# Kernel tuning notes

Measured on AMD Instinct MI355X. Metric: run time of the kernel, lower is better.

Reference implementation:

```python
import jax, jax.numpy as jnp
import numpy as np

EPS = 1e-8

def setup_inputs() -> dict:
    key = jax.random.key(0)
    k1, k2 = jax.random.split(key)
    B, N, D, K = 8, 8192, 768, 256
    x = jax.random.normal(k1, (B, N, D), dtype=jnp.float32)
    centers = jax.random.normal(k2, (B, K, D), dtype=jnp.float32)
    return {"x": x, "centers": centers}

def reference(x, centers):
    # tokens_norm / centers_norm as in the torch module (add-eps normalization)
    tn = x / (jnp.linalg.norm(x, axis=-1, keepdims=True) + EPS)
    cn = centers / (jnp.linalg.norm(centers, axis=-1, keepdims=True) + EPS)
    # F.cosine_similarity re-normalizes with clamp(norm, min=eps)
    tn2 = tn / jnp.maximum(jnp.linalg.norm(tn, axis=-1, keepdims=True), EPS)
    cn2 = cn / jnp.maximum(jnp.linalg.norm(cn, axis=-1, keepdims=True), EPS)
    # fused: cosine similarity via plain matmul instead of (B,N,K,D) broadcast
    cos_sim = jnp.einsum('bnd,bkd->bnk', tn2, cn2)  # (B,N,K)
    dist = 1.0 - cos_sim
    prob = jax.nn.softmax(-dist, axis=-1)  # softmax over K
    # weighted aggregation over N: (B,K,D)
    num = jnp.einsum('bnk,bnd->bkd', prob, x)
    den = jnp.sum(prob, axis=1)[..., None] + EPS  # (B,K,1)
    return num / den
```

## Files before the change

### kernel.cpp

```cpp
#include <hip/hip_runtime.h>
#include <hip/hip_bf16.h>

typedef __attribute__((ext_vector_type(8))) short bf16x8;
typedef __attribute__((ext_vector_type(4))) float f32x4;
typedef unsigned short u16;
typedef unsigned int u32;

__device__ __forceinline__ u16 f2bf(float f) {
    u32 u = __float_as_uint(f);
    u = (u + 0x7FFFu + ((u >> 16) & 1u)) >> 16;
    return (u16)u;
}
__device__ __forceinline__ u32 pk2(float a, float b) {
    return (u32)f2bf(a) | ((u32)f2bf(b) << 16);
}

#define GLDS16(g, l) __builtin_amdgcn_global_load_lds( \
    (const __attribute__((address_space(1))) u32*)(g), \
    (__attribute__((address_space(3))) u32*)(l), 16, 0, 0)

__global__ __launch_bounds__(256) void k_centers(const float* __restrict__ c, u16* __restrict__ cn) {
    int bid = blockIdx.x;
    int w = threadIdx.x >> 6, lane = threadIdx.x & 63;
    int row = (bid << 2) + w;
    int b = row >> 8;
    __shared__ u16 rb[4][800];
    const float* src = c + (size_t)row * 768;
    float v[12]; float ss = 0.f;
#pragma unroll
    for (int j = 0; j < 12; ++j) { v[j] = src[lane + (j << 6)]; ss += v[j] * v[j]; }
#pragma unroll
    for (int m = 1; m < 64; m <<= 1) ss += __shfl_xor(ss, m, 64);
    float inv = 1.0f / sqrtf(ss);
#pragma unroll
    for (int j = 0; j < 12; ++j) rb[w][lane + (j << 6)] = f2bf(v[j] * inv);
    __syncthreads();
    int t = threadIdx.x;
    int k0 = (bid << 2) & 255;
#pragma unroll
    for (int p = 0; p < 2; ++p) {
        int idx = (p << 8) + t;
        if (idx < 384) {
            int g = idx >> 2, kr = idx & 3;
            uint4 val = *reinterpret_cast<const uint4*>(&rb[kr][g << 3]);
            int kb = g >> 2, dc = g & 3;
            size_t o = ((((size_t)(b * 24 + kb) << 2) + dc) << 8) + k0 + kr;
            *reinterpret_cast<uint4*>(cn + (o << 3)) = val;
        }
    }
}

__global__ __launch_bounds__(256, 2) void k_gemm1(const float* __restrict__ x, const u16* __restrict__ cn,
                                                  u16* __restrict__ probT, float* __restrict__ den) {
    const int b = blockIdx.y;
    const int n0 = blockIdx.x << 7;
    const int t = threadIdx.x;
    const int wave = t >> 6, lane = t & 63;
    const int lg = lane >> 4, lr = lane & 15;
    const int wm = wave >> 1, wk = wave & 1;
    const int tok0 = wm << 6;
    const int kb0 = wk << 7;

    __shared__ union {
        struct {
            u16 A[2][4][130][8];
            u16 B[2][4][256][8];
        } s;
        u16 T[256][136];
    } u;
    __shared__ float inv_s[128];
    __shared__ float ksum[2][128];
    __shared__ float denp[256];

    denp[t] = 0.f;

    f32x4 acc[8][4];
#pragma unroll
    for (int kf = 0; kf < 8; ++kf)
#pragma unroll
        for (int tf = 0; tf < 4; ++tf) acc[kf][tf] = (f32x4){0.f, 0.f, 0.f, 0.f};

    const char* cnb = (const char*)(cn + (size_t)b * 24 * 4 * 256 * 8);
    const int tokS = ((t >> 1) & 63) + ((t >> 7) << 6);
    const int dcS = t & 1;
    const float* ap = x + ((size_t)b * 8192 + n0 + tokS) * 768 + (dcS << 3);

    float sq = 0.f;
    float4 f0, f1, f2, f3;

    auto issueA = [&](int kb) {
        const float* p = ap + (kb << 5);
        f0 = *reinterpret_cast<const float4*>(p);
        f1 = *reinterpret_cast<const float4*>(p + 4);
        f2 = *reinterpret_cast<const float4*>(p + 16);
        f3 = *reinterpret_cast<const float4*>(p + 20);
    };
    auto writeA = [&](int buf) {
        sq += f0.x*f0.x + f0.y*f0.y + f0.z*f0.z + f0.w*f0.w
            + f1.x*f1.x + f1.y*f1.y + f1.z*f1.z + f1.w*f1.w
            + f2.x*f2.x + f2.y*f2.y + f2.z*f2.z + f2.w*f2.w
            + f3.x*f3.x + f3.y*f3.y + f3.z*f3.z + f3.w*f3.w;
        *reinterpret_cast<uint4*>(&u.s.A[buf][dcS][tokS][0]) =
            make_uint4(pk2(f0.x, f0.y), pk2(f0.z, f0.w), pk2(f1.x, f1.y), pk2(f1.z, f1.w));
        *reinterpret_cast<uint4*>(&u.s.A[buf][dcS + 2][tokS][0]) =
            make_uint4(pk2(f2.x, f2.y), pk2(f2.z, f2.w), pk2(f3.x, f3.y), pk2(f3.z, f3.w));
    };
    auto issueB = [&](int buf, int kb) {
        const char* src = cnb + (size_t)kb * 16384 + (wave << 12) + (lane << 4);
        char* dst = (char*)&u.s.B[buf][0][0][0] + (wave << 12);
        GLDS16(src, dst);
        GLDS16(src + 1024, dst + 1024);
        GLDS16(src + 2048, dst + 2048);
        GLDS16(src + 3072, dst + 3072);
    };

    issueA(0); issueB(0, 0);
    writeA(0);
    __syncthreads();

    for (int kb = 0; kb < 24; ++kb) {
        int cur = kb & 1, nxt = cur ^ 1;
        if (kb < 23) { issueA(kb + 1); issueB(nxt, kb + 1); }
        bf16x8 a[4];
#pragma unroll
        for (int tf = 0; tf < 4; ++tf)
            a[tf] = *reinterpret_cast<const bf16x8*>(&u.s.A[cur][lg][tok0 + (tf << 4) + lr][0]);
#pragma unroll
        for (int kf = 0; kf < 8; ++kf) {
            bf16x8 bb = *reinterpret_cast<const bf16x8*>(&u.s.B[cur][lg][kb0 + (kf << 4) + lr][0]);
#pragma unroll
            for (int tf = 0; tf < 4; ++tf)
                acc[kf][tf] = __builtin_amdgcn_mfma_f32_16x16x32_bf16(a[tf], bb, acc[kf][tf], 0, 0, 0);
        }
        if (kb < 23) writeA(nxt);
        __syncthreads();
    }

    sq += __shfl_xor(sq, 1, 64);
    if ((t & 1) == 0) inv_s[tokS] = 1.0f / sqrtf(sq);
    __syncthreads();

    float iv[4][4];
#pragma unroll
    for (int tf = 0; tf < 4; ++tf)
#pragma unroll
        for (int r = 0; r < 4; ++r)
            iv[tf][r] = inv_s[tok0 + (tf << 4) + (lg << 2) + r];

    float rowsum[4][4];
#pragma unroll
    for (int tf = 0; tf < 4; ++tf)
#pragma unroll
        for (int r = 0; r < 4; ++r) rowsum[tf][r] = 0.f;
#pragma unroll
    for (int kf = 0; kf < 8; ++kf)
#pragma unroll
        for (int tf = 0; tf < 4; ++tf)
#pragma unroll
            for (int r = 0; r < 4; ++r) {
                float e = __expf(acc[kf][tf][r] * iv[tf][r]);
                acc[kf][tf][r] = e; rowsum[tf][r] += e;
            }
#pragma unroll
    for (int tf = 0; tf < 4; ++tf)
#pragma unroll
        for (int r = 0; r < 4; ++r) {
#pragma unroll
            for (int m = 1; m < 16; m <<= 1) rowsum[tf][r] += __shfl_xor(rowsum[tf][r], m, 64);
        }
    if (lr == 0) {
#pragma unroll
        for (int tf = 0; tf < 4; ++tf)
#pragma unroll
            for (int r = 0; r < 4; ++r)
                ksum[wk][tok0 + (tf << 4) + (lg << 2) + r] = rowsum[tf][r];
    }
    __syncthreads();

    float rs[4][4];
#pragma unroll
    for (int tf = 0; tf < 4; ++tf)
#pragma unroll
        for (int r = 0; r < 4; ++r) {
            int idx = tok0 + (tf << 4) + (lg << 2) + r;
            rs[tf][r] = 1.0f / (ksum[0][idx] + ksum[1][idx]);
        }

    float dcol[8];
#pragma unroll
    for (int kf = 0; kf < 8; ++kf) dcol[kf] = 0.f;
#pragma unroll
    for (int kf = 0; kf < 8; ++kf)
#pragma unroll
        for (int tf = 0; tf < 4; ++tf)
#pragma unroll
            for (int r = 0; r < 4; ++r) {
                float p = acc[kf][tf][r] * rs[tf][r];
                acc[kf][tf][r] = p; dcol[kf] += p;
            }
#pragma unroll
    for (int kf = 0; kf < 8; ++kf) {
        dcol[kf] += __shfl_xor(dcol[kf], 16, 64);
        dcol[kf] += __shfl_xor(dcol[kf], 32, 64);
    }
    if (lg == 0) {
#pragma unroll
        for (int kf = 0; kf < 8; ++kf) atomicAdd(&denp[kb0 + (kf << 4) + lr], dcol[kf]);
    }
#pragma unroll
    for (int kf = 0; kf < 8; ++kf)
#pragma unroll
        for (int tf = 0; tf < 4; ++tf)
            *reinterpret_cast<ushort4*>(&u.T[kb0 + (kf << 4) + lr][tok0 + (tf << 4) + (lg << 2)]) =
                make_ushort4(f2bf(acc[kf][tf][0]), f2bf(acc[kf][tf][1]),
                             f2bf(acc[kf][tf][2]), f2bf(acc[kf][tf][3]));
    __syncthreads();

    u16* pTb = probT + (size_t)b * 256 * 8192 + n0;
#pragma unroll
    for (int i = 0; i < 16; ++i) {
        int idx = (i << 8) + t;
        int row = idx >> 4, ch = idx & 15;
        *reinterpret_cast<uint4*>(pTb + (size_t)row * 8192 + (ch << 3)) =
            *reinterpret_cast<const uint4*>(&u.T[row][ch << 3]);
    }
    atomicAdd(&den[(b << 8) + t], denp[t]);
}

__global__ __launch_bounds__(256) void k_gemm2(const float* __restrict__ x, const u16* __restrict__ probT,
                                               float* __restrict__ num_part) {
    const int bid = blockIdx.x;
    const int xcd = bid & 7, slot = bid >> 3;
    const int orig = xcd * 96 + slot;
    const int dt = orig % 12, sb = orig / 12;
    const int s = sb >> 3, b = sb & 7;
    const int d0 = dt << 6;
    const int t = threadIdx.x;
    const int wave = t >> 6, lane = t & 63;
    const int lg = lane >> 4, lr = lane & 15;

    f32x4 acc[4][4];
#pragma unroll
    for (int m = 0; m < 4; ++m)
#pragma unroll
        for (int tt = 0; tt < 4; ++tt) acc[m][tt] = (f32x4){0.f, 0.f, 0.f, 0.f};

    const int n0 = s << 10;
    const u16* pA = probT + (size_t)b * 256 * 8192;
    const float* xB = x + (size_t)b * 8192 * 768;

    for (int kb = 0; kb < 32; ++kb) {
        int nbase = n0 + (kb << 5);
        bf16x8 a[4];
#pragma unroll
        for (int m = 0; m < 4; ++m) {
            int k = (wave << 6) + (m << 4) + lr;
            a[m] = *reinterpret_cast<const bf16x8*>(pA + (size_t)k * 8192 + nbase + (lg << 3));
        }
        const float* xr = xB + (size_t)(nbase + (lg << 3)) * 768 + d0 + lr;
        bf16x8 bb[4];
#pragma unroll
        for (int tt = 0; tt < 4; ++tt)
#pragma unroll
            for (int j = 0; j < 8; ++j) {
                float f = xr[(size_t)j * 768 + (tt << 4)];
                bb[tt][j] = (short)f2bf(f);
            }
#pragma unroll
        for (int m = 0; m < 4; ++m)
#pragma unroll
            for (int tt = 0; tt < 4; ++tt)
                acc[m][tt] = __builtin_amdgcn_mfma_f32_16x16x32_bf16(a[m], bb[tt], acc[m][tt], 0, 0, 0);
    }

    float* np = num_part + ((size_t)s * 8 + b) * 256 * 768;
#pragma unroll
    for (int m = 0; m < 4; ++m) {
        int kb_ = (wave << 6) + (m << 4) + (lg << 2);
#pragma unroll
        for (int reg = 0; reg < 4; ++reg)
#pragma unroll
            for (int tt = 0; tt < 4; ++tt)
                np[(size_t)(kb_ + reg) * 768 + d0 + (tt << 4) + lr] = acc[m][tt][reg];
    }
}

__global__ __launch_bounds__(256) void k_final(const float* __restrict__ num_part, const float* __restrict__ den,
                                               float* __restrict__ out) {
    int i = blockIdx.x * 256 + threadIdx.x;
    float sum = 0.f;
#pragma unroll
    for (int ss = 0; ss < 8; ++ss) sum += num_part[(size_t)ss * 1572864 + i];
    out[i] = sum / (den[i / 768] + 1e-8f);
}

extern "C" void kernel_launch(void* const* d_in, const int* in_sizes, int n_in,
                              void* d_out, int out_size, void* d_ws, size_t ws_size,
                              hipStream_t stream) {
    const float* x = (const float*)d_in[0];
    const float* centers = (const float*)d_in[1];
    float* out = (float*)d_out;
    char* ws = (char*)d_ws;
    u16* cn       = (u16*)ws;
    u16* probT    = (u16*)(ws + 3145728);
    float* den    = (float*)(ws + 36700160);
    float* numpt  = (float*)(ws + 36708352);

    hipMemsetAsync(den, 0, 8192, stream);
    k_centers<<<512, 256, 0, stream>>>(centers, cn);
    k_gemm1<<<dim3(64, 8), 256, 0, stream>>>(x, cn, probT, den);
    k_gemm2<<<768, 256, 0, stream>>>(x, probT, numpt);
    k_final<<<6144, 256, 0, stream>>>(numpt, den, out);
}
```

Measured before the change: 177.8 us.

## Fuse split-N reduction and normalization into gemm2 via atomic adds to output

Drops the partial-sum buffer and the final reduction kernel. gemm2 now scales its accumulators by the reciprocal of the denominator and atomically adds them straight into the output. The output and den zeroing move into k_centers, which removes the memset launch. This saves two launches and the round trip of writing and re-reading partial sums, at the cost of float atomics, contention across the 8 N-splits, and a summation order that is not deterministic.

```diff
diff --git a/kernel.cpp b/kernel.cpp
--- a/kernel.cpp
+++ b/kernel.cpp
@@ -19,11 +19,19 @@
     (const __attribute__((address_space(1))) u32*)(g), \
     (__attribute__((address_space(3))) u32*)(l), 16, 0, 0)
 
-__global__ __launch_bounds__(256) void k_centers(const float* __restrict__ c, u16* __restrict__ cn) {
+__global__ __launch_bounds__(256) void k_centers(const float* __restrict__ c, u16* __restrict__ cn,
+                                                 float* __restrict__ den, float* __restrict__ out) {
     int bid = blockIdx.x;
     int w = threadIdx.x >> 6, lane = threadIdx.x & 63;
     int row = (bid << 2) + w;
     int b = row >> 8;
+    if (bid < 8) den[(bid << 8) + threadIdx.x] = 0.f;
+    {
+        float4* o4 = reinterpret_cast<float4*>(out) + (size_t)bid * 768 + threadIdx.x;
+        o4[0] = float4{0.f, 0.f, 0.f, 0.f};
+        o4[256] = float4{0.f, 0.f, 0.f, 0.f};
+        o4[512] = float4{0.f, 0.f, 0.f, 0.f};
+    }
     __shared__ u16 rb[4][800];
     const float* src = c + (size_t)row * 768;
     float v[12]; float ss = 0.f;
@@ -228,7 +236,7 @@
 }
 
 __global__ __launch_bounds__(256) void k_gemm2(const float* __restrict__ x, const u16* __restrict__ probT,
-                                               float* __restrict__ num_part) {
+                                               const float* __restrict__ den, float* __restrict__ out) {
     const int bid = blockIdx.x;
     const int xcd = bid & 7, slot = bid >> 3;
     const int orig = xcd * 96 + slot;
@@ -273,25 +281,19 @@
                 acc[m][tt] = __builtin_amdgcn_mfma_f32_16x16x32_bf16(a[m], bb[tt], acc[m][tt], 0, 0, 0);
     }
 
-    float* np = num_part + ((size_t)s * 8 + b) * 256 * 768;
+    float* ob = out + (size_t)(b << 8) * 768;
 #pragma unroll
     for (int m = 0; m < 4; ++m) {
         int kb_ = (wave << 6) + (m << 4) + (lg << 2);
 #pragma unroll
-        for (int reg = 0; reg < 4; ++reg)
+        for (int reg = 0; reg < 4; ++reg) {
+            float dv = 1.0f / (den[(b << 8) + kb_ + reg] + 1e-8f);
 #pragma unroll
             for (int tt = 0; tt < 4; ++tt)
-                np[(size_t)(kb_ + reg) * 768 + d0 + (tt << 4) + lr] = acc[m][tt][reg];
-    }
-}
-
-__global__ __launch_bounds__(256) void k_final(const float* __restrict__ num_part, const float* __restrict__ den,
-                                               float* __restrict__ out) {
-    int i = blockIdx.x * 256 + threadIdx.x;
-    float sum = 0.f;
-#pragma unroll
-    for (int ss = 0; ss < 8; ++ss) sum += num_part[(size_t)ss * 1572864 + i];
-    out[i] = sum / (den[i / 768] + 1e-8f);
+                unsafeAtomicAdd(&ob[(size_t)(kb_ + reg) * 768 + d0 + (tt << 4) + lr],
+                                acc[m][tt][reg] * dv);
+        }
+    }
 }
 
 extern "C" void kernel_launch(void* const* d_in, const int* in_sizes, int n_in,
@@ -304,11 +306,8 @@
     u16* cn       = (u16*)ws;
     u16* probT    = (u16*)(ws + 3145728);
     float* den    = (float*)(ws + 36700160);
-    float* numpt  = (float*)(ws + 36708352);
-
-    hipMemsetAsync(den, 0, 8192, stream);
-    k_centers<<<512, 256, 0, stream>>>(centers, cn);
+
+    k_centers<<<512, 256, 0, stream>>>(centers, cn, den, out);
     k_gemm1<<<dim3(64, 8), 256, 0, stream>>>(x, cn, probT, den);
-    k_gemm2<<<768, 256, 0, stream>>>(x, probT, numpt);
-    k_final<<<6144, 256, 0, stream>>>(numpt, den, out);
-}
+    k_gemm2<<<768, 256, 0, stream>>>(x, probT, den, out);
+}
```

Measured after the change: 164.4 us. -7.5%, faster.
